# Kernel tuning notes

Hardware: AMD Instinct MI355X
Metric: run time of the kernel (lower is better)

## Reference

```python
import jax, jax.numpy as jnp
import numpy as np


def setup_inputs() -> dict:
    key = jax.random.key(0)
    k1, k2 = jax.random.split(key)
    B, D = 1048576, 16
    model_out = jax.random.normal(k1, (B, D), dtype=jnp.float32)
    y_true = jax.random.normal(k2, (B, D), dtype=jnp.float32)
    return {"model_out": model_out, "y_true": y_true}


def _elem_loss(x, y):
    # nn.MSELoss(reduction='none'): elementwise squared error
    return (x - y) ** 2


def reference(model_out, y_true):
    # loss: [B, D] elementwise
    loss = _elem_loss(model_out, y_true)

    # d_loss = d(loss.sum())/d(model_out), same shape as model_out
    d_loss = jax.grad(lambda x: _elem_loss(x, y_true).sum())(model_out)

    # sqd_loss[b, i, j] = d^2 loss / d x[b,i] d x[b,j].
    # Loss is elementwise (no cross-batch coupling), so the Hessian is
    # block-diagonal over batch: compute a [D, D] per-sample Hessian via
    # vmap(jacfwd(grad)) instead of the torch per-dim autograd loop.
    def per_sample_grad(x_b, y_b):  # [D] -> [D]
        return jax.grad(lambda x: _elem_loss(x, y_b).sum())(x_b)

    sqd_loss = jax.vmap(
        lambda x_b, y_b: jax.jacfwd(per_sample_grad)(x_b, y_b)
    )(model_out, y_true)  # [B, D, D]

    return loss, d_loss, sqd_loss
```

## Files before the change

### kernel.cpp

```cpp
#include <hip/hip_runtime.h>


__global__ __launch_bounds__(256) void loss_grad_kernel(
    const float4* __restrict__ x,
    const float4* __restrict__ y,
    float4* __restrict__ loss,
    float4* __restrict__ dloss,
    int n4) {
    int i = blockIdx.x * blockDim.x + threadIdx.x;
    if (i >= n4) return;
    float4 a = x[i];
    float4 b = y[i];
    float4 d;
    d.x = a.x - b.x;
    d.y = a.y - b.y;
    d.z = a.z - b.z;
    d.w = a.w - b.w;
    float4 l;
    l.x = d.x * d.x;
    l.y = d.y * d.y;
    l.z = d.z * d.z;
    l.w = d.w * d.w;
    float4 g;
    g.x = 2.0f * d.x;
    g.y = 2.0f * d.y;
    g.z = 2.0f * d.z;
    g.w = 2.0f * d.w;
    loss[i] = l;
    dloss[i] = g;
}

__global__ __launch_bounds__(256) void hess_fill_kernel(
    float4* __restrict__ out, unsigned int n4) {
    unsigned int i = blockIdx.x * blockDim.x + threadIdx.x;
    if (i >= n4) return;
    unsigned int f = i << 2;
    unsigned int col = f & 15u;
    unsigned int row = (f >> 4) & 15u;
    float4 v;
    v.x = (row == col)      ? 2.0f : 0.0f;
    v.y = (row == col + 1u) ? 2.0f : 0.0f;
    v.z = (row == col + 2u) ? 2.0f : 0.0f;
    v.w = (row == col + 3u) ? 2.0f : 0.0f;
    out[i] = v;
}

extern "C" void kernel_launch(void* const* d_in, const int* in_sizes, int n_in,
                              void* d_out, int out_size, void* d_ws, size_t ws_size,
                              hipStream_t stream) {
    const float* model_out = (const float*)d_in[0];
    const float* y_true    = (const float*)d_in[1];
    float* out = (float*)d_out;

    const int BD = in_sizes[0];
    float* loss_p  = out;
    float* dloss_p = out + BD;
    float* sqd_p   = out + 2 * (size_t)BD;

    {
        int n4 = BD / 4;
        int block = 256;
        int grid = (n4 + block - 1) / block;
        loss_grad_kernel<<<grid, block, 0, stream>>>(
            (const float4*)model_out, (const float4*)y_true,
            (float4*)loss_p, (float4*)dloss_p, n4);
    }

    {
        unsigned int n4 = (unsigned int)((size_t)BD * 16 / 4);
        int block = 256;
        unsigned int grid = (n4 + block - 1) / block;
        hess_fill_kernel<<<grid, block, 0, stream>>>((float4*)sqd_p, n4);
    }
}
```

Baseline: 1.232 ms.

## Fuse loss/grad and Hessian fill into one grid-stride kernel with nontemporal stores

Merges the elementwise loss/gradient kernel and the constant Hessian fill kernel into a single persistent grid-stride kernel with a fixed grid of 2048 blocks. The Hessian pattern value is computed once per thread, which works because the stride is a multiple of 64 float4s, so each thread's pattern never changes. All outputs use nontemporal stores to avoid polluting caches with streamed write-only data. This removes one launch and per-element index math, but the fixed grid size may underfill or serialize work compared to one thread per element.

Result: slower. 1.306 ms (+6.0%).

```diff
diff --git a/kernel.cpp b/kernel.cpp
--- a/kernel.cpp
+++ b/kernel.cpp
@@ -1,48 +1,41 @@
 #include <hip/hip_runtime.h>
 
 
-__global__ __launch_bounds__(256) void loss_grad_kernel(
-    const float4* __restrict__ x,
-    const float4* __restrict__ y,
-    float4* __restrict__ loss,
-    float4* __restrict__ dloss,
-    int n4) {
-    int i = blockIdx.x * blockDim.x + threadIdx.x;
-    if (i >= n4) return;
-    float4 a = x[i];
-    float4 b = y[i];
-    float4 d;
-    d.x = a.x - b.x;
-    d.y = a.y - b.y;
-    d.z = a.z - b.z;
-    d.w = a.w - b.w;
-    float4 l;
-    l.x = d.x * d.x;
-    l.y = d.y * d.y;
-    l.z = d.z * d.z;
-    l.w = d.w * d.w;
-    float4 g;
-    g.x = 2.0f * d.x;
-    g.y = 2.0f * d.y;
-    g.z = 2.0f * d.z;
-    g.w = 2.0f * d.w;
-    loss[i] = l;
-    dloss[i] = g;
-}
+typedef float vfloat4 __attribute__((ext_vector_type(4)));
 
-__global__ __launch_bounds__(256) void hess_fill_kernel(
-    float4* __restrict__ out, unsigned int n4) {
-    unsigned int i = blockIdx.x * blockDim.x + threadIdx.x;
-    if (i >= n4) return;
-    unsigned int f = i << 2;
-    unsigned int col = f & 15u;
-    unsigned int row = (f >> 4) & 15u;
-    float4 v;
+__global__ __launch_bounds__(256) void fused_autograd_kernel(
+    const vfloat4* __restrict__ x,
+    const vfloat4* __restrict__ y,
+    vfloat4* __restrict__ loss,
+    vfloat4* __restrict__ dloss,
+    vfloat4* __restrict__ sqd,
+    unsigned int loss_n4,
+    unsigned int hess_n4) {
+    const unsigned int tid    = blockIdx.x * blockDim.x + threadIdx.x;
+    const unsigned int stride = gridDim.x * blockDim.x;
+
+    for (unsigned int i = tid; i < loss_n4; i += stride) {
+        vfloat4 a = x[i];
+        vfloat4 b = y[i];
+        vfloat4 d = a - b;
+        vfloat4 l = d * d;
+        vfloat4 g = d + d;
+        __builtin_nontemporal_store(l, &loss[i]);
+        __builtin_nontemporal_store(g, &dloss[i]);
+    }
+
+    const unsigned int f   = (tid << 2) & 255u;
+    const unsigned int col = f & 15u;
+    const unsigned int row = (f >> 4) & 15u;
+    vfloat4 v;
     v.x = (row == col)      ? 2.0f : 0.0f;
     v.y = (row == col + 1u) ? 2.0f : 0.0f;
     v.z = (row == col + 2u) ? 2.0f : 0.0f;
     v.w = (row == col + 3u) ? 2.0f : 0.0f;
-    out[i] = v;
+
+    for (unsigned int i = tid; i < hess_n4; i += stride) {
+        __builtin_nontemporal_store(v, &sqd[i]);
+    }
 }
 
 extern "C" void kernel_launch(void* const* d_in, const int* in_sizes, int n_in,
@@ -57,19 +50,14 @@
     float* dloss_p = out + BD;
     float* sqd_p   = out + 2 * (size_t)BD;
 
-    {
-        int n4 = BD / 4;
-        int block = 256;
-        int grid = (n4 + block - 1) / block;
-        loss_grad_kernel<<<grid, block, 0, stream>>>(
-            (const float4*)model_out, (const float4*)y_true,
-            (float4*)loss_p, (float4*)dloss_p, n4);
-    }
+    const unsigned int loss_n4 = (unsigned int)(BD / 4);
+    const unsigned int hess_n4 = (unsigned int)((size_t)BD * 16 / 4);
 
-    {
-        unsigned int n4 = (unsigned int)((size_t)BD * 16 / 4);
-        int block = 256;
-        unsigned int grid = (n4 + block - 1) / block;
-        hess_fill_kernel<<<grid, block, 0, stream>>>((float4*)sqd_p, n4);
-    }
+    const int block = 256;
+    const int grid  = 2048;
+
+    fused_autograd_kernel<<<grid, block, 0, stream>>>(
+        (const vfloat4*)model_out, (const vfloat4*)y_true,
+        (vfloat4*)loss_p, (vfloat4*)dloss_p, (vfloat4*)sqd_p,
+        loss_n4, hess_n4);
 }
```
